# Kernel tuning notes

Measured on AMD Instinct MI355X. Metric: run time of the kernel, lower is better.

Reference implementation:

```python
import jax, jax.numpy as jnp
import numpy as np

N_NODES = 50000
N_EDGES = 1600000
N_GRAPHS = 512
VOCAB = 1000
EMB = 32
HID = 64
N_CLASS = 2


def setup_inputs() -> dict:
    key = jax.random.key(0)
    ks = jax.random.split(key, 12)
    x_ids = jax.random.randint(ks[0], (N_NODES,), 0, VOCAB)
    edge_index = jax.random.randint(ks[1], (2, N_EDGES), 0, N_NODES)
    batch = jnp.sort(jax.random.randint(ks[2], (N_NODES,), 0, N_GRAPHS))
    def s(k, shape, fan):
        return jax.random.normal(k, shape, jnp.float32) * (1.0 / np.sqrt(fan))
    return {
        "x_ids": x_ids,
        "edge_index": edge_index,
        "batch": batch,
        "embed": s(ks[3], (VOCAB, EMB), EMB),
        "w1_l": s(ks[4], (EMB, HID), EMB),
        "b1": jnp.zeros((HID,), jnp.float32),
        "w1_r": s(ks[5], (EMB, HID), EMB),
        "w2_l": s(ks[6], (HID, HID), HID),
        "b2": jnp.zeros((HID,), jnp.float32),
        "w2_r": s(ks[7], (HID, HID), HID),
        "w_out": s(ks[8], (HID, N_CLASS), HID),
        "b_out": jnp.zeros((N_CLASS,), jnp.float32),
    }


def _sage(x, src, dst, w_l, b, w_r):
    # PyG SAGEConv (aggr='mean'): out = lin_l(mean_{j in N(i)} x_j) + lin_r(x_i)
    msg_sum = jax.ops.segment_sum(x[src], dst, num_segments=N_NODES)  # [N, d]
    deg = jax.ops.segment_sum(jnp.ones((src.shape[0],), x.dtype), dst,
                              num_segments=N_NODES)
    mean = msg_sum / jnp.maximum(deg, 1.0)[:, None]
    return mean @ w_l + b + x @ w_r


def reference(x_ids, edge_index, batch, embed, w1_l, b1, w1_r,
              w2_l, b2, w2_r, w_out, b_out):
    src, dst = edge_index[0], edge_index[1]
    x = embed[x_ids]                                  # [N, emb]
    x = jax.nn.relu(_sage(x, src, dst, w1_l, b1, w1_r))  # [N, hid]
    x = jax.nn.relu(_sage(x, src, dst, w2_l, b2, w2_r))  # [N, hid]
    # global_mean_pool over batch segments
    gsum = jax.ops.segment_sum(x, batch, num_segments=N_GRAPHS)
    gcnt = jax.ops.segment_sum(jnp.ones((N_NODES,), x.dtype), batch,
                               num_segments=N_GRAPHS)
    pooled = gsum / jnp.maximum(gcnt, 1.0)[:, None]   # [G, hid]
    return pooled @ w_out + b_out                     # [G, n_class]
```

## Files before the change

kernel.cpp:

```cpp
#include <hip/hip_runtime.h>
#include <hip/hip_bf16.h>

#define N_NODES 50000
#define N_EDGES 1600000
#define N_GRAPHS 512
#define VOCAB 1000
#define EMB 32
#define HID 64
#define N_CLASS 2

#define MAXDEG 96

#define NVEC (N_EDGES / 4)
#define SORT_VPB 1024
#define SORT_EPB (SORT_VPB * 4)
#define SORT_BLOCKS ((NVEC + SORT_VPB - 1) / SORT_VPB)
#define BSHIFT 7
#define BUCKET_NODES 128
#define NBUCK ((N_NODES + BUCKET_NODES - 1) / BUCKET_NODES)

#define E1_BLOCKS ((VOCAB * HID + 255) / 256)

#define AGG_THREADS (N_NODES * 8)
#define AGG_BLOCKS ((AGG_THREADS + 255) / 256)

#define L2P_BLOCKS 768
#define L2P_WAVES (L2P_BLOCKS * 4)
#define L2P_CHUNK ((N_NODES + L2P_WAVES - 1) / L2P_WAVES)

typedef int iv4 __attribute__((ext_vector_type(4)));
typedef unsigned short us;
typedef us usv8 __attribute__((ext_vector_type(8)));
typedef float fv4 __attribute__((ext_vector_type(4)));
typedef unsigned long long u64;

__device__ __forceinline__ float bf2f(us u) {
    union { unsigned int i; float f; } c;
    c.i = ((unsigned int)u) << 16;
    return c.f;
}
__device__ __forceinline__ us f2bf(float f) {
    union { __hip_bfloat16 b; us u; } c;
    c.b = __float2bfloat16(f);
    return c.u;
}
__device__ __forceinline__ float rdlane(float v, int k) {
    return __int_as_float(__builtin_amdgcn_readlane(__float_as_int(v), k));
}

__global__ __launch_bounds__(256) void pre_hist_kernel(
        const int* __restrict__ dst, int* __restrict__ hist,
        const float* __restrict__ embed, const float* __restrict__ w1l,
        const float* __restrict__ w1r, us* __restrict__ e1b,
        float* __restrict__ e1r) {
    __shared__ int lh[NBUCK];
    if (blockIdx.x < SORT_BLOCKS) {
        for (int b = threadIdx.x; b < NBUCK; b += 256) lh[b] = 0;
        __syncthreads();
        const iv4* dst4 = (const iv4*)dst;
        int vbase = blockIdx.x * SORT_VPB;
        #pragma unroll
        for (int t = 0; t < 4; ++t) {
            int v = vbase + t * 256 + threadIdx.x;
            if (v < NVEC) {
                iv4 d4 = __builtin_nontemporal_load(&dst4[v]);
                atomicAdd(&lh[d4.x >> BSHIFT], 1);
                atomicAdd(&lh[d4.y >> BSHIFT], 1);
                atomicAdd(&lh[d4.z >> BSHIFT], 1);
                atomicAdd(&lh[d4.w >> BSHIFT], 1);
            }
        }
        __syncthreads();
        for (int b = threadIdx.x; b < NBUCK; b += 256)
            hist[b * SORT_BLOCKS + blockIdx.x] = lh[b];
    } else {
        int id = (blockIdx.x - SORT_BLOCKS) * 256 + threadIdx.x;
        if (id >= VOCAB * HID) return;
        int v = id >> 6, j = id & 63;
        float a = 0.0f, b = 0.0f;
        #pragma unroll
        for (int k = 0; k < EMB; ++k) {
            float ev = embed[v * EMB + k];
            a = fmaf(ev, w1l[k * HID + j], a);
            b = fmaf(ev, w1r[k * HID + j], b);
        }
        e1b[id] = f2bf(a);
        e1r[id] = b;
    }
}

__global__ __launch_bounds__(256) void scan_rows_kernel(int* __restrict__ hist,
                                                        int* __restrict__ btot) {
    int* row = hist + (size_t)blockIdx.x * SORT_BLOCKS;
    __shared__ int wsum[4];
    int tid = threadIdx.x, lane = tid & 63, w = tid >> 6;
    int carry = 0;
    for (int base = 0; base < SORT_BLOCKS; base += 256) {
        int idx = base + tid;
        int v = (idx < SORT_BLOCKS) ? row[idx] : 0;
        int inc = v;
        #pragma unroll
        for (int off = 1; off < 64; off <<= 1) {
            int n = __shfl_up(inc, off, 64);
            if (lane >= off) inc += n;
        }
        if (lane == 63) wsum[w] = inc;
        __syncthreads();
        int woff = 0;
        #pragma unroll
        for (int k = 0; k < 4; ++k) if (k < w) woff += wsum[k];
        if (idx < SORT_BLOCKS) row[idx] = carry + woff + inc - v;
        carry += wsum[0] + wsum[1] + wsum[2] + wsum[3];
        __syncthreads();
    }
    if (tid == 0) btot[blockIdx.x] = carry;
}

__global__ __launch_bounds__(256) void scatter_kernel(const int* __restrict__ src,
        const int* __restrict__ dst, const int* __restrict__ x_ids,
        const int* __restrict__ hist, const int* __restrict__ btot,
        int* __restrict__ boff, u64* __restrict__ ebuf) {
    __shared__ u64 ebuf_l[SORT_EPB];
    __shared__ int lh[NBUCK];
    __shared__ int lstart[NBUCK];
    __shared__ int lcur[NBUCK];
    __shared__ int wsum[4];
    int tid = threadIdx.x, lane = tid & 63, w = tid >> 6;
    int blk = blockIdx.x;

    const iv4* dst4 = (const iv4*)dst;
    const iv4* src4 = (const iv4*)src;
    int vbase = blk * SORT_VPB;
    iv4 d4s[4], s4s[4];
    bool vok[4];
    #pragma unroll
    for (int t = 0; t < 4; ++t) {
        int v = vbase + t * 256 + tid;
        vok[t] = (v < NVEC);
        if (vok[t]) {
            d4s[t] = __builtin_nontemporal_load(&dst4[v]);
            s4s[t] = __builtin_nontemporal_load(&src4[v]);
        }
    }

    for (int b = tid; b < NBUCK; b += 256) lh[b] = 0;
    __syncthreads();
    #pragma unroll
    for (int t = 0; t < 4; ++t) {
        if (vok[t]) {
            atomicAdd(&lh[d4s[t].x >> BSHIFT], 1);
            atomicAdd(&lh[d4s[t].y >> BSHIFT], 1);
            atomicAdd(&lh[d4s[t].z >> BSHIFT], 1);
            atomicAdd(&lh[d4s[t].w >> BSHIFT], 1);
        }
    }
    __syncthreads();

    int carry = 0;
    for (int base = 0; base < NBUCK; base += 256) {
        int idx = base + tid;
        int v = (idx < NBUCK) ? lh[idx] : 0;
        int inc = v;
        #pragma unroll
        for (int off = 1; off < 64; off <<= 1) {
            int n = __shfl_up(inc, off, 64);
            if (lane >= off) inc += n;
        }
        if (lane == 63) wsum[w] = inc;
        __syncthreads();
        int woff = 0;
        #pragma unroll
        for (int k = 0; k < 4; ++k) if (k < w) woff += wsum[k];
        if (idx < NBUCK) {
            int ex = carry + woff + inc - v;
            lstart[idx] = ex;
            lcur[idx] = ex;
        }
        carry += wsum[0] + wsum[1] + wsum[2] + wsum[3];
        __syncthreads();
    }
    int total = carry;

    #pragma unroll
    for (int t = 0; t < 4; ++t) {
        if (vok[t]) {
            iv4 d4 = d4s[t], s4 = s4s[t];
            int pay0 = (x_ids[s4.x] << 16) | s4.x;
            int pay1 = (x_ids[s4.y] << 16) | s4.y;
            int pay2 = (x_ids[s4.z] << 16) | s4.z;
            int pay3 = (x_ids[s4.w] << 16) | s4.w;
            int p0 = atomicAdd(&lcur[d4.x >> BSHIFT], 1);
            int p1 = atomicAdd(&lcur[d4.y >> BSHIFT], 1);
            int p2 = atomicAdd(&lcur[d4.z >> BSHIFT], 1);
            int p3 = atomicAdd(&lcur[d4.w >> BSHIFT], 1);
            ebuf_l[p0] = ((u64)(unsigned)d4.x << 32) | (unsigned)pay0;
            ebuf_l[p1] = ((u64)(unsigned)d4.y << 32) | (unsigned)pay1;
            ebuf_l[p2] = ((u64)(unsigned)d4.z << 32) | (unsigned)pay2;
            ebuf_l[p3] = ((u64)(unsigned)d4.w << 32) | (unsigned)pay3;
        }
    }
    __syncthreads();

    carry = 0;
    for (int base = 0; base < NBUCK; base += 256) {
        int idx = base + tid;
        int v = (idx < NBUCK) ? btot[idx] : 0;
        int inc = v;
        #pragma unroll
        for (int off = 1; off < 64; off <<= 1) {
            int n = __shfl_up(inc, off, 64);
            if (lane >= off) inc += n;
        }
        if (lane == 63) wsum[w] = inc;
        __syncthreads();
        int woff = 0;
        #pragma unroll
        for (int k = 0; k < 4; ++k) if (k < w) woff += wsum[k];
        if (idx < NBUCK) {
            int gb = carry + woff + inc - v;
            if (blk == 0) boff[idx] = gb;
            lh[idx] = gb + hist[idx * SORT_BLOCKS + blk] - lstart[idx];
        }
        carry += wsum[0] + wsum[1] + wsum[2] + wsum[3];
        __syncthreads();
    }
    if (blk == 0 && tid == 0) boff[NBUCK] = carry;
    __syncthreads();

    for (int i = tid; i < total; i += 256) {
        u64 e = ebuf_l[i];
        int b = (int)(e >> (32 + BSHIFT));
        ebuf[lh[b] + i] = e;
    }
}

__global__ __launch_bounds__(256) void csr_bucket_kernel(const u64* __restrict__ ebuf,
        const int* __restrict__ boff, int* __restrict__ cursor, int* __restrict__ csr,
        float* __restrict__ gsum) {
    int b = blockIdx.x;
    int tid = threadIdx.x;
    __shared__ int cur[BUCKET_NODES];
    for (int r = tid; r < BUCKET_NODES; r += 256) cur[r] = 0;
    if (b < 128) gsum[b * 256 + tid] = 0.0f;
    __syncthreads();
    int base = boff[b];
    int end  = boff[b + 1];
    int node0 = b << BSHIFT;
    for (int i = base + tid; i < end; i += 256) {
        u64 e = ebuf[i];
        int d = (int)(e >> 32);
        int pay = (int)(e & 0xffffffffu);
        int pos = atomicAdd(&cur[d - node0], 1);
        csr[(size_t)d * MAXDEG + pos] = pay;
    }
    __syncthreads();
    for (int r = tid; r < BUCKET_NODES; r += 256) {
        int d = node0 + r;
        if (d < N_NODES) cursor[d] = cur[r];
    }
}

__global__ __launch_bounds__(256) void agg1_lin1_kernel(
        const int* __restrict__ x_ids, const int* __restrict__ csr,
        const int* __restrict__ deg_arr, const us* __restrict__ e1b,
        const float* __restrict__ e1r, const float* __restrict__ b1,
        us* __restrict__ h1b) {
    int tid = blockIdx.x * blockDim.x + threadIdx.x;
    int lane = threadIdx.x & 63;
    int g = lane >> 3, c8 = lane & 7;
    int node = (tid >> 6) * 8 + g;
    bool valid = node < N_NODES;
    int nclamp = valid ? node : 0;
    int deg = valid ? deg_arr[nclamp] : 0;
    const int* crow = csr + (size_t)nclamp * MAXDEG;
    float a0=0.f,a1=0.f,a2=0.f,a3=0.f,a4=0.f,a5=0.f,a6=0.f,a7=0.f;
    for (int k = 0; k < deg; k += 4) {
        iv4 cv = *(const iv4*)(crow + k);
        #define GATH1(CVAL, T)                                                   \
        if (k + (T) < deg) {                                                     \
            int cls = (CVAL) >> 16;                                              \
            usv8 r = *(const usv8*)(e1b + cls * HID + c8 * 8);                   \
            a0 += bf2f(r[0]); a1 += bf2f(r[1]); a2 += bf2f(r[2]); a3 += bf2f(r[3]); \
            a4 += bf2f(r[4]); a5 += bf2f(r[5]); a6 += bf2f(r[6]); a7 += bf2f(r[7]); \
        }
        GATH1(cv.x, 0) GATH1(cv.y, 1) GATH1(cv.z, 2) GATH1(cv.w, 3)
        #undef GATH1
    }
    if (!valid) return;
    float inv = 1.0f / fmaxf((float)deg, 1.0f);
    int xid = x_ids[nclamp];
    const fv4* er = (const fv4*)(e1r + xid * HID + c8 * 8);
    fv4 e0 = er[0], e1v = er[1];
    const fv4* bb = (const fv4*)(b1 + c8 * 8);
    fv4 b0 = bb[0], b1v = bb[1];
    float h0 = fmaxf(a0 * inv + b0.x + e0.x, 0.0f);
    float h1 = fmaxf(a1 * inv + b0.y + e0.y, 0.0f);
    float h2 = fmaxf(a2 * inv + b0.z + e0.z, 0.0f);
    float h3 = fmaxf(a3 * inv + b0.w + e0.w, 0.0f);
    float h4 = fmaxf(a4 * inv + b1v.x + e1v.x, 0.0f);
    float h5 = fmaxf(a5 * inv + b1v.y + e1v.y, 0.0f);
    float h6 = fmaxf(a6 * inv + b1v.z + e1v.z, 0.0f);
    float h7 = fmaxf(a7 * inv + b1v.w + e1v.w, 0.0f);
    int o = node * HID + c8 * 8;
    usv8 hb;
    hb[0] = f2bf(h0); hb[1] = f2bf(h1); hb[2] = f2bf(h2); hb[3] = f2bf(h3);
    hb[4] = f2bf(h4); hb[5] = f2bf(h5); hb[6] = f2bf(h6); hb[7] = f2bf(h7);
    *(usv8*)(h1b + o) = hb;
}

__global__ __launch_bounds__(256) void agg2_mean_kernel(
        const us* __restrict__ h1b, const int* __restrict__ csr,
        const int* __restrict__ deg_arr, us* __restrict__ mean2b) {
    int tid = blockIdx.x * blockDim.x + threadIdx.x;
    int lane = threadIdx.x & 63;
    int g = lane >> 3, c8 = lane & 7;
    int node = (tid >> 6) * 8 + g;
    bool valid = node < N_NODES;
    int nclamp = valid ? node : 0;
    int deg = valid ? deg_arr[nclamp] : 0;
    const int* crow = csr + (size_t)nclamp * MAXDEG;
    float a0=0.f,a1=0.f,a2=0.f,a3=0.f,a4=0.f,a5=0.f,a6=0.f,a7=0.f;
    for (int k = 0; k < deg; k += 4) {
        iv4 cv = *(const iv4*)(crow + k);
        #define GATH2(CVAL, T)                                                   \
        if (k + (T) < deg) {                                                     \
            int nb = (CVAL) & 0xFFFF;                                            \
            usv8 r = *(const usv8*)(h1b + nb * HID + c8 * 8);                    \
            a0 += bf2f(r[0]); a1 += bf2f(r[1]); a2 += bf2f(r[2]); a3 += bf2f(r[3]); \
            a4 += bf2f(r[4]); a5 += bf2f(r[5]); a6 += bf2f(r[6]); a7 += bf2f(r[7]); \
        }
        GATH2(cv.x, 0) GATH2(cv.y, 1) GATH2(cv.z, 2) GATH2(cv.w, 3)
        #undef GATH2
    }
    if (!valid) return;
    float inv = 1.0f / fmaxf((float)deg, 1.0f);
    int o = node * HID + c8 * 8;
    usv8 mb;
    mb[0] = f2bf(a0 * inv); mb[1] = f2bf(a1 * inv);
    mb[2] = f2bf(a2 * inv); mb[3] = f2bf(a3 * inv);
    mb[4] = f2bf(a4 * inv); mb[5] = f2bf(a5 * inv);
    mb[6] = f2bf(a6 * inv); mb[7] = f2bf(a7 * inv);
    *(usv8*)(mean2b + o) = mb;
}

__global__ __launch_bounds__(256) void lin2_pool_kernel(
        const us* __restrict__ mean2b, const us* __restrict__ h1b,
        const float* __restrict__ w2l, const float* __restrict__ b2,
        const float* __restrict__ w2r, const int* __restrict__ batch,
        float* __restrict__ gsum) {
    int lane = threadIdx.x & 63;
    int wv = (blockIdx.x * blockDim.x + threadIdx.x) >> 6;
    int i0 = wv * L2P_CHUNK;
    int i1 = i0 + L2P_CHUNK; if (i1 > N_NODES) i1 = N_NODES;
    if (i0 >= N_NODES) return;
    float wl[HID], wr[HID];
    #pragma unroll
    for (int k = 0; k < HID; ++k) {
        wl[k] = w2l[k * HID + lane];
        wr[k] = w2r[k * HID + lane];
    }
    float bj = b2[lane];
    int curg = __builtin_amdgcn_readfirstlane(batch[i0]);
    float accp = 0.0f;
    float m = bf2f(mean2b[i0 * HID + lane]);
    float h = bf2f(h1b[i0 * HID + lane]);
    for (int i = i0; i < i1; ++i) {
        us mn_u = 0, hn_u = 0;
        if (i + 1 < i1) {
            mn_u = mean2b[(i + 1) * HID + lane];
            hn_u = h1b[(i + 1) * HID + lane];
        }
        int g = __builtin_amdgcn_readfirstlane(batch[i]);
        if (g != curg) {
            atomicAdd(&gsum[curg * HID + lane], accp);
            accp = 0.0f;
            curg = g;
        }
        float zm = 0.0f, zh = bj;
        #pragma unroll
        for (int k = 0; k < HID; ++k) {
            zm = fmaf(rdlane(m, k), wl[k], zm);
            zh = fmaf(rdlane(h, k), wr[k], zh);
        }
        accp += fmaxf(zm + zh, 0.0f);
        m = bf2f(mn_u); h = bf2f(hn_u);
    }
    atomicAdd(&gsum[curg * HID + lane], accp);
}

__global__ void out_kernel(const float* __restrict__ gsum, const int* __restrict__ batch,
                           const float* __restrict__ w_out, const float* __restrict__ b_out,
                           float* __restrict__ out) {
    int id = blockIdx.x * blockDim.x + threadIdx.x;
    if (id >= N_GRAPHS * N_CLASS) return;
    int g = id >> 1, c = id & 1;
    int lo = 0, hi = N_NODES;
    while (lo < hi) { int mid = (lo + hi) >> 1; if (batch[mid] < g) lo = mid + 1; else hi = mid; }
    int first = lo;
    lo = 0; hi = N_NODES;
    while (lo < hi) { int mid = (lo + hi) >> 1; if (batch[mid] <= g) lo = mid + 1; else hi = mid; }
    float cnt = (float)(lo - first);
    float inv = 1.0f / fmaxf(cnt, 1.0f);
    float acc = b_out[c];
    #pragma unroll
    for (int j = 0; j < HID; ++j)
        acc = fmaf(gsum[g * HID + j] * inv, w_out[j * N_CLASS + c], acc);
    out[id] = acc;
}


extern "C" void kernel_launch(void* const* d_in, const int* in_sizes, int n_in,
                              void* d_out, int out_size, void* d_ws, size_t ws_size,
                              hipStream_t stream) {
    const int*   x_ids = (const int*)d_in[0];
    const int*   edge  = (const int*)d_in[1];
    const int*   batch = (const int*)d_in[2];
    const float* embed = (const float*)d_in[3];
    const float* w1l   = (const float*)d_in[4];
    const float* b1    = (const float*)d_in[5];
    const float* w1r   = (const float*)d_in[6];
    const float* w2l   = (const float*)d_in[7];
    const float* b2    = (const float*)d_in[8];
    const float* w2r   = (const float*)d_in[9];
    const float* wout  = (const float*)d_in[10];
    const float* bout  = (const float*)d_in[11];
    const int* src = edge;
    const int* dst = edge + N_EDGES;
    float* out = (float*)d_out;

    char* ws = (char*)d_ws;
    size_t off = 0;
    auto alloc = [&](size_t bytes) -> void* {
        void* p = ws + off;
        off += (bytes + 255) & ~(size_t)255;
        return p;
    };
    us*     h1b    = (us*)alloc((size_t)N_NODES * HID * 2);
    u64*    ebuf   = (u64*)alloc((size_t)N_EDGES * 8);
    int*    csr    = (int*)alloc((size_t)N_NODES * MAXDEG * 4);
    int*    cursor = (int*)alloc((size_t)N_NODES * 4);
    int*    hist   = (int*)alloc((size_t)NBUCK * SORT_BLOCKS * 4);
    int*    btot   = (int*)alloc((size_t)NBUCK * 4);
    int*    boff   = (int*)alloc((size_t)(NBUCK + 1) * 4);
    us*     e1b    = (us*)alloc((size_t)VOCAB * HID * 2);
    float*  e1r    = (float*)alloc((size_t)VOCAB * HID * 4);
    float*  gsum   = (float*)alloc((size_t)N_GRAPHS * HID * 4);

    us* mean2b = (us*)ebuf;

    const int B = 256;
    pre_hist_kernel<<<SORT_BLOCKS + E1_BLOCKS, B, 0, stream>>>(dst, hist,
                                                               embed, w1l, w1r, e1b, e1r);
    scan_rows_kernel<<<NBUCK, B, 0, stream>>>(hist, btot);
    scatter_kernel<<<SORT_BLOCKS, B, 0, stream>>>(src, dst, x_ids, hist, btot, boff, ebuf);
    csr_bucket_kernel<<<NBUCK, B, 0, stream>>>(ebuf, boff, cursor, csr, gsum);
    agg1_lin1_kernel<<<AGG_BLOCKS, B, 0, stream>>>(x_ids, csr, cursor,
                                                   e1b, e1r, b1, h1b);
    agg2_mean_kernel<<<AGG_BLOCKS, B, 0, stream>>>(h1b, csr, cursor, mean2b);
    lin2_pool_kernel<<<L2P_BLOCKS, B, 0, stream>>>(mean2b, h1b, w2l, b2, w2r, batch, gsum);
    out_kernel<<<(N_GRAPHS * N_CLASS + B - 1) / B, B, 0, stream>>>(gsum, batch, wout, bout, out);
}
```

Measured before the change: 200.9 us.

## Pack sorted edges into 32 bits and stage CSR rows in shared memory

The bucket scatter now stores each edge as a 32-bit word (bucket id, local destination node, source) instead of a 64-bit pair, which halves the global edge-buffer traffic. The x_ids lookup moves from the scatter kernel into the CSR build kernel. That kernel now fills a per-bucket shared-memory slab and writes the CSR rows out in a coalesced pass rather than scattering global writes. In exchange it uses about 48KB of LDS per block, which may lower occupancy, and the packing assumes node ids fit in 16 bits.

After: 201.1 us. Within noise of the previous version (+0.1%).

```diff
diff --git a/kernel.cpp b/kernel.cpp
--- a/kernel.cpp
+++ b/kernel.cpp
@@ -32,7 +32,7 @@
 typedef unsigned short us;
 typedef us usv8 __attribute__((ext_vector_type(8)));
 typedef float fv4 __attribute__((ext_vector_type(4)));
-typedef unsigned long long u64;
+typedef unsigned int u32;
 
 __device__ __forceinline__ float bf2f(us u) {
     union { unsigned int i; float f; } c;
@@ -117,10 +117,10 @@
 }
 
 __global__ __launch_bounds__(256) void scatter_kernel(const int* __restrict__ src,
-        const int* __restrict__ dst, const int* __restrict__ x_ids,
+        const int* __restrict__ dst,
         const int* __restrict__ hist, const int* __restrict__ btot,
-        int* __restrict__ boff, u64* __restrict__ ebuf) {
-    __shared__ u64 ebuf_l[SORT_EPB];
+        int* __restrict__ boff, u32* __restrict__ ebuf) {
+    __shared__ u32 ebuf_l[SORT_EPB];
     __shared__ int lh[NBUCK];
     __shared__ int lstart[NBUCK];
     __shared__ int lcur[NBUCK];
@@ -185,18 +185,14 @@
     for (int t = 0; t < 4; ++t) {
         if (vok[t]) {
             iv4 d4 = d4s[t], s4 = s4s[t];
-            int pay0 = (x_ids[s4.x] << 16) | s4.x;
-            int pay1 = (x_ids[s4.y] << 16) | s4.y;
-            int pay2 = (x_ids[s4.z] << 16) | s4.z;
-            int pay3 = (x_ids[s4.w] << 16) | s4.w;
-            int p0 = atomicAdd(&lcur[d4.x >> BSHIFT], 1);
-            int p1 = atomicAdd(&lcur[d4.y >> BSHIFT], 1);
-            int p2 = atomicAdd(&lcur[d4.z >> BSHIFT], 1);
-            int p3 = atomicAdd(&lcur[d4.w >> BSHIFT], 1);
-            ebuf_l[p0] = ((u64)(unsigned)d4.x << 32) | (unsigned)pay0;
-            ebuf_l[p1] = ((u64)(unsigned)d4.y << 32) | (unsigned)pay1;
-            ebuf_l[p2] = ((u64)(unsigned)d4.z << 32) | (unsigned)pay2;
-            ebuf_l[p3] = ((u64)(unsigned)d4.w << 32) | (unsigned)pay3;
+            #define PLACE(D, S) {                                                \
+                int b_ = (D) >> BSHIFT;                                          \
+                int p_ = atomicAdd(&lcur[b_], 1);                                \
+                ebuf_l[p_] = ((u32)b_ << 23) | ((u32)((D) & (BUCKET_NODES-1)) << 16) \
+                           | (u32)(S);                                           \
+            }
+            PLACE(d4.x, s4.x) PLACE(d4.y, s4.y) PLACE(d4.z, s4.z) PLACE(d4.w, s4.w)
+            #undef PLACE
         }
     }
     __syncthreads();
@@ -228,18 +224,19 @@
     __syncthreads();
 
     for (int i = tid; i < total; i += 256) {
-        u64 e = ebuf_l[i];
-        int b = (int)(e >> (32 + BSHIFT));
-        ebuf[lh[b] + i] = e;
-    }
-}
-
-__global__ __launch_bounds__(256) void csr_bucket_kernel(const u64* __restrict__ ebuf,
-        const int* __restrict__ boff, int* __restrict__ cursor, int* __restrict__ csr,
-        float* __restrict__ gsum) {
+        u32 e = ebuf_l[i];
+        int b = (int)(e >> 23);
+        ebuf[lh[b] + i] = e & 0x7FFFFFu;
+    }
+}
+
+__global__ __launch_bounds__(256) void csr_bucket_kernel(const u32* __restrict__ ebuf,
+        const int* __restrict__ boff, const int* __restrict__ x_ids,
+        int* __restrict__ cursor, int* __restrict__ csr, float* __restrict__ gsum) {
+    __shared__ int slab[BUCKET_NODES * MAXDEG];
+    __shared__ int cur[BUCKET_NODES];
     int b = blockIdx.x;
     int tid = threadIdx.x;
-    __shared__ int cur[BUCKET_NODES];
     for (int r = tid; r < BUCKET_NODES; r += 256) cur[r] = 0;
     if (b < 128) gsum[b * 256 + tid] = 0.0f;
     __syncthreads();
@@ -247,16 +244,23 @@
     int end  = boff[b + 1];
     int node0 = b << BSHIFT;
     for (int i = base + tid; i < end; i += 256) {
-        u64 e = ebuf[i];
-        int d = (int)(e >> 32);
-        int pay = (int)(e & 0xffffffffu);
-        int pos = atomicAdd(&cur[d - node0], 1);
-        csr[(size_t)d * MAXDEG + pos] = pay;
+        u32 e = ebuf[i];
+        int r = (int)(e >> 16);
+        int s = (int)(e & 0xFFFFu);
+        int pay = (x_ids[s] << 16) | s;
+        int pos = atomicAdd(&cur[r], 1);
+        slab[r * MAXDEG + pos] = pay;
     }
     __syncthreads();
     for (int r = tid; r < BUCKET_NODES; r += 256) {
         int d = node0 + r;
         if (d < N_NODES) cursor[d] = cur[r];
+    }
+    int* crow = csr + (size_t)node0 * MAXDEG;
+    for (int j = tid; j < BUCKET_NODES * MAXDEG; j += 256) {
+        int r = j / MAXDEG;
+        int p = j - r * MAXDEG;
+        if (p < cur[r]) crow[j] = slab[j];
     }
 }
 
@@ -436,7 +440,7 @@
         return p;
     };
     us*     h1b    = (us*)alloc((size_t)N_NODES * HID * 2);
-    u64*    ebuf   = (u64*)alloc((size_t)N_EDGES * 8);
+    u32*    ebuf   = (u32*)alloc((size_t)N_EDGES * 4);
     int*    csr    = (int*)alloc((size_t)N_NODES * MAXDEG * 4);
     int*    cursor = (int*)alloc((size_t)N_NODES * 4);
     int*    hist   = (int*)alloc((size_t)NBUCK * SORT_BLOCKS * 4);
@@ -452,8 +456,8 @@
     pre_hist_kernel<<<SORT_BLOCKS + E1_BLOCKS, B, 0, stream>>>(dst, hist,
                                                                embed, w1l, w1r, e1b, e1r);
     scan_rows_kernel<<<NBUCK, B, 0, stream>>>(hist, btot);
-    scatter_kernel<<<SORT_BLOCKS, B, 0, stream>>>(src, dst, x_ids, hist, btot, boff, ebuf);
-    csr_bucket_kernel<<<NBUCK, B, 0, stream>>>(ebuf, boff, cursor, csr, gsum);
+    scatter_kernel<<<SORT_BLOCKS, B, 0, stream>>>(src, dst, hist, btot, boff, ebuf);
+    csr_bucket_kernel<<<NBUCK, B, 0, stream>>>(ebuf, boff, x_ids, cursor, csr, gsum);
     agg1_lin1_kernel<<<AGG_BLOCKS, B, 0, stream>>>(x_ids, csr, cursor,
                                                    e1b, e1r, b1, h1b);
     agg2_mean_kernel<<<AGG_BLOCKS, B, 0, stream>>>(h1b, csr, cursor, mean2b);
```
